# Kernel tuning notes

Hardware: AMD Instinct MI355X
Metric: run time of the kernel (lower is better)

Reference implementation:

```python
import jax, jax.numpy as jnp
import numpy as np

B, S, Hd, NH, FF = 4, 2048, 1024, 16, 4096
D = Hd // NH  # head size 64
EPS = 1e-12


def _ln(x, g, b):
    mu = jnp.mean(x, axis=-1, keepdims=True)
    var = jnp.mean(jnp.square(x - mu), axis=-1, keepdims=True)
    return (x - mu) * jax.lax.rsqrt(var + EPS) * g + b


def _rope(q, k):
    # q,k: [B,NH,S,D]; RoFormer interleaved rotary
    inv = 1.0 / (10000.0 ** (jnp.arange(0, D, 2, dtype=jnp.float32) / D))
    freqs = jnp.arange(S, dtype=jnp.float32)[:, None] * inv[None, :]  # [S,D/2]
    cos = jnp.repeat(jnp.cos(freqs), 2, axis=-1)  # [S,D]
    sin = jnp.repeat(jnp.sin(freqs), 2, axis=-1)

    def rot(x):  # [x0,x1,x2,x3,...] -> [-x1,x0,-x3,x2,...]
        return jnp.stack([-x[..., 1::2], x[..., 0::2]], axis=-1).reshape(x.shape)

    return q * cos + rot(q) * sin, k * cos + rot(k) * sin


def setup_inputs() -> dict:
    key = jax.random.key(0)
    ks = jax.random.split(key, 12)
    s = 0.02
    return {
        "x": jax.random.normal(ks[0], (B, S, Hd), jnp.float32),
        "Wq": jax.random.normal(ks[1], (Hd, Hd), jnp.float32) * s,
        "bq": jnp.zeros((Hd,), jnp.float32),
        "Wk": jax.random.normal(ks[2], (Hd, Hd), jnp.float32) * s,
        "bk": jnp.zeros((Hd,), jnp.float32),
        "Wv": jax.random.normal(ks[3], (Hd, Hd), jnp.float32) * s,
        "bv": jnp.zeros((Hd,), jnp.float32),
        "Wo": jax.random.normal(ks[4], (Hd, Hd), jnp.float32) * s,
        "bo": jnp.zeros((Hd,), jnp.float32),
        "g1": jnp.ones((Hd,), jnp.float32),
        "beta1": jnp.zeros((Hd,), jnp.float32),
        "W1": jax.random.normal(ks[5], (Hd, FF), jnp.float32) * s,
        "b1": jnp.zeros((FF,), jnp.float32),
        "W2": jax.random.normal(ks[6], (FF, Hd), jnp.float32) * s,
        "b2": jnp.zeros((Hd,), jnp.float32),
        "g2": jnp.ones((Hd,), jnp.float32),
        "beta2": jnp.zeros((Hd,), jnp.float32),
    }


def reference(x, Wq, bq, Wk, bk, Wv, bv, Wo, bo, g1, beta1, W1, b1, W2, b2, g2, beta2):
    def proj(W, b):  # [B,S,Hd] -> [B,NH,S,D]
        return (x @ W + b).reshape(B, S, NH, D).transpose(0, 2, 1, 3)

    q, k, v = proj(Wq, bq), proj(Wk, bk), proj(Wv, bv)
    q, k = _rope(q, k)
    scores = jnp.einsum('bhqd,bhkd->bhqk', q, k) / jnp.sqrt(jnp.float32(D))
    attn = jax.nn.softmax(scores, axis=-1)
    ctx = jnp.einsum('bhqk,bhkd->bhqd', attn, v)
    ctx = ctx.transpose(0, 2, 1, 3).reshape(B, S, Hd)
    attn_out = ctx @ Wo + bo
    h = _ln(x + attn_out, g1, beta1)
    ffn = jax.nn.gelu(h @ W1 + b1) @ W2 + b2
    return _ln(h + ffn, g2, beta2)
```

## Files before the change

### kernel.cpp

```cpp
#include <hip/hip_runtime.h>

#define BB   4
#define SS   2048
#define HD   1024
#define NHH  16
#define DD   64
#define FFF  4096
#define BS   (BB*SS)
#define BHN  (BB*NHH)

typedef __attribute__((ext_vector_type(8))) short v8s;
typedef __attribute__((ext_vector_type(4))) short v4s;
typedef __attribute__((ext_vector_type(4))) float v4f;

__device__ __forceinline__ short f2bf(float f) {
    union { float f; unsigned u; } v; v.f = f;
    unsigned r = (v.u + 0x7fffu + ((v.u >> 16) & 1u)) >> 16;
    return (short)r;
}
__device__ __forceinline__ unsigned pack2bf(float a, float b) {
    return (unsigned)(unsigned short)f2bf(a) | ((unsigned)(unsigned short)f2bf(b) << 16);
}
__device__ __forceinline__ float bf2f(short s) {
    union { unsigned u; float f; } v; v.u = ((unsigned)(unsigned short)s) << 16;
    return v.f;
}
__device__ __forceinline__ v4f mfma16(v8s a, v8s b, v4f c) {
    return __builtin_amdgcn_mfma_f32_16x16x32_bf16(a, b, c, 0, 0, 0);
}
__device__ __forceinline__ void cp16(void* lds, const void* g) {
    __builtin_amdgcn_global_load_lds(
        (const __attribute__((address_space(1))) unsigned*)g,
        (__attribute__((address_space(3))) unsigned*)lds, 16, 0, 0);
}


__global__ __launch_bounds__(256) void cast_bf16(const float* __restrict__ X,
                                                 short* __restrict__ Y, int n) {
    const int i = (blockIdx.x * 256 + threadIdx.x) * 4;
    if (i < n) {
        const float4 v = *(const float4*)(X + i);
        v4s o = { f2bf(v.x), f2bf(v.y), f2bf(v.z), f2bf(v.w) };
        *(v4s*)(Y + i) = o;
    }
}

__global__ __launch_bounds__(256) void rope_tab(float* __restrict__ C, float* __restrict__ Sn) {
    const int i = blockIdx.x * 256 + threadIdx.x;
    const int s = i >> 5, di = i & 31;
    const float inv = powf(10000.f, -(float)(2 * di) * (1.f / 64.f));
    const float a = (float)s * inv;
    C[i]  = cosf(a);
    Sn[i] = sinf(a);
}

__global__ __launch_bounds__(256) void transW(const float* __restrict__ W,
                                              short* __restrict__ WT, int K, int N) {
    __shared__ float T[64][65];
    const int t = threadIdx.x;
    const int r0 = blockIdx.y * 64, c0 = blockIdx.x * 64;
#pragma unroll
    for (int i = 0; i < 4; i++) {
        const int lin = t + 256 * i;
        const int r = lin >> 4, c = (lin & 15) * 4;
        const float4 v = *(const float4*)(W + (size_t)(r0 + r) * N + c0 + c);
        T[r][c] = v.x; T[r][c+1] = v.y; T[r][c+2] = v.z; T[r][c+3] = v.w;
    }
    __syncthreads();
#pragma unroll
    for (int i = 0; i < 4; i++) {
        const int lin = t + 256 * i;
        const int n = lin >> 4, k = (lin & 15) * 4;
        v4s o = { f2bf(T[k][n]), f2bf(T[k+1][n]), f2bf(T[k+2][n]), f2bf(T[k+3][n]) };
        *(v4s*)(WT + (size_t)(c0 + n) * K + r0 + k) = o;
    }
}

__global__ __launch_bounds__(256) void transV(const short* __restrict__ Vh,
                                              short* __restrict__ Vt) {
    __shared__ short T[64][72];
    const int bh = blockIdx.y, s0 = blockIdx.x * 64;
    const int t = threadIdx.x;
    const short* src = Vh + ((size_t)bh * SS + s0) * DD;
#pragma unroll
    for (int i = 0; i < 4; i++) {
        const int lin = t + 256 * i;
        const int r = lin >> 4, c = (lin & 15) * 4;
        const v4s v = *(const v4s*)(src + (size_t)r * DD + c);
        T[r][c] = v[0]; T[r][c+1] = v[1]; T[r][c+2] = v[2]; T[r][c+3] = v[3];
    }
    __syncthreads();
    short* dst = Vt + (size_t)bh * DD * SS;
#pragma unroll
    for (int i = 0; i < 4; i++) {
        const int lin = t + 256 * i;
        const int d = lin >> 4, sg = (lin & 15) * 4;
        v4s o = { T[sg][d], T[sg+1][d], T[sg+2][d], T[sg+3][d] };
        *(v4s*)(dst + (size_t)d * SS + s0 + sg) = o;
    }
}


template <int EPI>
__global__ __launch_bounds__(256, 2) void gemm_bt(
    const short* __restrict__ A, const short* __restrict__ Bt,
    const float* __restrict__ bias, const float* __restrict__ bias2,
    const float* __restrict__ bias3, void* __restrict__ out,
    const void* __restrict__ resid,
    const float* __restrict__ ropeC, const float* __restrict__ ropeS,
    int M, int N, int K, float oscale)
{
    __shared__ short As[128 * 32];
    __shared__ short Bs[128 * 32];
    const int t = threadIdx.x;
    const int wave = t >> 6, lane = t & 63;
    const int quad = lane >> 4, l16 = lane & 15;
    const int wm = wave & 1, wn = wave >> 1;
    const int m0 = blockIdx.x * 128, n0 = blockIdx.y * 128;

    v4f acc[4][4];
#pragma unroll
    for (int i = 0; i < 4; i++)
#pragma unroll
        for (int j = 0; j < 4; j++) { v4f z = {0.f, 0.f, 0.f, 0.f}; acc[i][j] = z; }

    const int r4 = lane >> 2;
    const int g4 = (lane & 3) ^ ((lane >> 3) & 3);
    const short* Asrc = A  + (size_t)(m0 + wave * 32 + r4) * K + g4 * 8;
    const short* Bsrc = Bt + (size_t)(n0 + wave * 32 + r4) * K + g4 * 8;
    short* Adst = As + wave * 1024;
    short* Bdst = Bs + wave * 1024;
    const int pshift = (l16 >> 1) & 3;

    for (int k0 = 0; k0 < K; k0 += 32) {
        __syncthreads();
        cp16(Adst,       Asrc + k0);
        cp16(Adst + 512, Asrc + (size_t)16 * K + k0);
        cp16(Bdst,       Bsrc + k0);
        cp16(Bdst + 512, Bsrc + (size_t)16 * K + k0);
        __syncthreads();
        v8s af[4], bfr[4];
#pragma unroll
        for (int i = 0; i < 4; i++)
            af[i] = *(const v8s*)(As + (wm * 64 + i * 16 + l16) * 32 + (quad ^ pshift) * 8);
#pragma unroll
        for (int j = 0; j < 4; j++)
            bfr[j] = *(const v8s*)(Bs + (wn * 64 + j * 16 + l16) * 32 + (quad ^ pshift) * 8);
#pragma unroll
        for (int i = 0; i < 4; i++)
#pragma unroll
            for (int j = 0; j < 4; j++)
                acc[i][j] = mfma16(af[i], bfr[j], acc[i][j]);
    }

#pragma unroll
    for (int j = 0; j < 4; j++) {
        const int col = n0 + wn * 64 + j * 16 + l16;
        float bval;
        if constexpr (EPI == 0) {
            const int h = col >> 10;
            const float* bp = (h == 0) ? bias : ((h == 1) ? bias2 : bias3);
            bval = bp[col & 1023];
        } else {
            bval = bias[col];
        }
#pragma unroll
        for (int i = 0; i < 4; i++) {
#pragma unroll
            for (int r = 0; r < 4; r++) {
                const int row = m0 + wm * 64 + i * 16 + quad * 4 + r;
                float v = acc[i][j][r] + bval;
                if constexpr (EPI == 0) {
                    const int h = col >> 10;
                    if (h == 0) v *= oscale;
                    const int s = row & (SS - 1);
                    const int d = col & 63;
                    float o = v;
                    if (h < 2) {
                        const float cv = ropeC[s * 32 + (d >> 1)];
                        const float sv = ropeS[s * 32 + (d >> 1)];
                        const float partner = __shfl_xor(v, 1);
                        o = (d & 1) ? fmaf(v, cv, partner * sv)
                                    : fmaf(v, cv, -partner * sv);
                    }
                    const int b_ = row >> 11, hh = (col >> 6) & 15;
                    ((short*)out)[(size_t)h * (BHN * SS * DD)
                                  + (((size_t)(b_ * NHH + hh)) * SS + s) * DD + d] = f2bf(o);
                } else if constexpr (EPI == 2) {
                    v += ((const float*)resid)[(size_t)row * N + col];
                    ((float*)out)[(size_t)row * N + col] = v;
                } else if constexpr (EPI == 3) {
                    const float tq = v * v;
                    const float u = v * fmaf(0.035677408136f, tq, 0.7978845608028654f);
                    const float e = __builtin_amdgcn_exp2f(-2.8853900817779268f * u);
                    const float g = v * __builtin_amdgcn_rcpf(1.f + e);
                    ((short*)out)[(size_t)row * N + col] = f2bf(g);
                } else {
                    v += bf2f(((const short*)resid)[(size_t)row * N + col]);
                    ((float*)out)[(size_t)row * N + col] = v;
                }
            }
        }
    }
}

__global__ __launch_bounds__(256, 3) void attn_kernel(
    const short* __restrict__ Qh, const short* __restrict__ Kh,
    const short* __restrict__ Vt, short* __restrict__ ctx)
{
    __shared__ short Ks[64 * 64];
    __shared__ short Vs[64 * 64];
    __shared__ short Ps[4][16 * 88];
    __shared__ float Li[4][32];
    const int bh = blockIdx.x, q0 = blockIdx.y * 128;
    const int t = threadIdx.x, wave = t >> 6, lane = t & 63;
    const int quad = lane >> 4, l16 = lane & 15;

    const short* qp = Qh + ((size_t)bh * SS + q0 + wave * 32 + l16) * DD;
    v8s bq[2][2];
    bq[0][0] = *(const v8s*)(qp + quad * 8);
    bq[0][1] = *(const v8s*)(qp + 32 + quad * 8);
    bq[1][0] = *(const v8s*)(qp + (size_t)16 * DD + quad * 8);
    bq[1][1] = *(const v8s*)(qp + (size_t)16 * DD + 32 + quad * 8);

    v4f o[2][4];
#pragma unroll
    for (int qs = 0; qs < 2; qs++)
#pragma unroll
        for (int c = 0; c < 4; c++) { v4f z = {0.f, 0.f, 0.f, 0.f}; o[qs][c] = z; }
    float li[2] = {0.f, 0.f};

    const short* Kb = Kh + (size_t)bh * SS * DD;
    const short* Vb = Vt + (size_t)bh * DD * SS;
    const int r8 = lane >> 3;
    const int g8 = (lane & 7) ^ (r8 & 7);
    short* Psw = (short*)Ps[wave];
    const int xsw = l16 & 7;

    for (int kt = 0; kt < SS; kt += 64) {
        __syncthreads();
        cp16(Ks + wave * 1024,       Kb + (size_t)(kt + wave * 16 + r8) * DD + g8 * 8);
        cp16(Ks + wave * 1024 + 512, Kb + (size_t)(kt + wave * 16 + 8 + r8) * DD + g8 * 8);
        cp16(Vs + wave * 1024,       Vb + (size_t)(wave * 16 + r8) * SS + kt + g8 * 8);
        cp16(Vs + wave * 1024 + 512, Vb + (size_t)(wave * 16 + 8 + r8) * SS + kt + g8 * 8);
        __syncthreads();

        v4f sc[2][4];
#pragma unroll
        for (int c = 0; c < 4; c++) {
            const v8s k0f = *(const v8s*)(Ks + (c * 16 + l16) * 64 + ((quad    ) ^ xsw) * 8);
            const v8s k1f = *(const v8s*)(Ks + (c * 16 + l16) * 64 + ((quad + 4) ^ xsw) * 8);
#pragma unroll
            for (int qs = 0; qs < 2; qs++) {
                v4f z = {0.f, 0.f, 0.f, 0.f};
                z = mfma16(k0f, bq[qs][0], z);
                z = mfma16(k1f, bq[qs][1], z);
                sc[qs][c] = z;
            }
        }

        v8s pa[2][2];
#pragma unroll
        for (int qs = 0; qs < 2; qs++) {
            float lp = 0.f;
#pragma unroll
            for (int c = 0; c < 4; c++) {
#pragma unroll
                for (int r = 0; r < 4; r++) {
                    const float p = __builtin_amdgcn_exp2f(sc[qs][c][r]);
                    sc[qs][c][r] = p;
                    lp += p;
                }
            }
            li[qs] += lp;
            short* pw = Psw + l16 * 88;
#pragma unroll
            for (int c = 0; c < 4; c++) {
                *(unsigned*)(pw + c * 16 + quad * 4)     = pack2bf(sc[qs][c][0], sc[qs][c][1]);
                *(unsigned*)(pw + c * 16 + quad * 4 + 2) = pack2bf(sc[qs][c][2], sc[qs][c][3]);
            }
            pa[qs][0] = *(const v8s*)(Psw + l16 * 88 + quad * 8);
            pa[qs][1] = *(const v8s*)(Psw + l16 * 88 + 32 + quad * 8);
        }

#pragma unroll
        for (int c = 0; c < 4; c++) {
            const v8s v0f = *(const v8s*)(Vs + (c * 16 + l16) * 64 + ((quad    ) ^ xsw) * 8);
            const v8s v1f = *(const v8s*)(Vs + (c * 16 + l16) * 64 + ((quad + 4) ^ xsw) * 8);
#pragma unroll
            for (int qs = 0; qs < 2; qs++) {
                o[qs][c] = mfma16(pa[qs][0], v0f, o[qs][c]);
                o[qs][c] = mfma16(pa[qs][1], v1f, o[qs][c]);
            }
        }
    }

    float linv[2][4];
#pragma unroll
    for (int qs = 0; qs < 2; qs++) {
        float lf = li[qs];
        lf += __shfl_xor(lf, 16);
        lf += __shfl_xor(lf, 32);
        if (quad == 0) Li[wave][qs * 16 + l16] = lf;
    }
    __builtin_amdgcn_s_barrier();
#pragma unroll
    for (int qs = 0; qs < 2; qs++) {
        const v4f lv = *(const v4f*)(&Li[wave][qs * 16 + quad * 4]);
#pragma unroll
        for (int r = 0; r < 4; r++) linv[qs][r] = __builtin_amdgcn_rcpf(lv[r]);
    }
    const int b_ = bh >> 4, h_ = bh & 15;
#pragma unroll
    for (int qs = 0; qs < 2; qs++)
#pragma unroll
        for (int c = 0; c < 4; c++)
#pragma unroll
            for (int r = 0; r < 4; r++) {
                const int s = q0 + wave * 32 + qs * 16 + quad * 4 + r;
                const int d = c * 16 + l16;
                ctx[((size_t)(b_ * SS + s)) * HD + h_ * DD + d] =
                    f2bf(o[qs][c][r] * linv[qs][r]);
            }
}

__global__ __launch_bounds__(256) void ln_kernel(
    const float* __restrict__ X, const float* __restrict__ g, const float* __restrict__ b,
    float* __restrict__ Y, short* __restrict__ Yb)
{
    const int row = blockIdx.x;
    const int t = threadIdx.x;
    const float4 v = *(const float4*)(X + (size_t)row * HD + t * 4);
    float s = v.x + v.y + v.z + v.w;
    float sq = v.x * v.x + v.y * v.y + v.z * v.z + v.w * v.w;
#pragma unroll
    for (int m = 1; m < 64; m <<= 1) { s += __shfl_xor(s, m); sq += __shfl_xor(sq, m); }
    __shared__ float red[8];
    const int wave = t >> 6, lane = t & 63;
    if (lane == 0) { red[wave] = s; red[4 + wave] = sq; }
    __syncthreads();
    s  = red[0] + red[1] + red[2] + red[3];
    sq = red[4] + red[5] + red[6] + red[7];
    const float mu = s * (1.f / HD);
    const float var = sq * (1.f / HD) - mu * mu;
    const float rs = rsqrtf(var + 1e-12f);
    const float4 gg = *(const float4*)(g + t * 4);
    const float4 bb = *(const float4*)(b + t * 4);
    const float y0 = (v.x - mu) * rs * gg.x + bb.x;
    const float y1 = (v.y - mu) * rs * gg.y + bb.y;
    const float y2 = (v.z - mu) * rs * gg.z + bb.z;
    const float y3 = (v.w - mu) * rs * gg.w + bb.w;
    if (Y)  { float4 o = { y0, y1, y2, y3 }; *(float4*)(Y + (size_t)row * HD + t * 4) = o; }
    if (Yb) { v4s o = { f2bf(y0), f2bf(y1), f2bf(y2), f2bf(y3) };
              *(v4s*)(Yb + (size_t)row * HD + t * 4) = o; }
}

extern "C" void kernel_launch(void* const* d_in, const int* in_sizes, int n_in,
                              void* d_out, int out_size, void* d_ws, size_t ws_size,
                              hipStream_t stream)
{
    (void)in_sizes; (void)n_in; (void)out_size;
    const float* x   = (const float*)d_in[0];
    const float* Wq  = (const float*)d_in[1];
    const float* bq  = (const float*)d_in[2];
    const float* Wk  = (const float*)d_in[3];
    const float* bk  = (const float*)d_in[4];
    const float* Wv  = (const float*)d_in[5];
    const float* bv  = (const float*)d_in[6];
    const float* Wo  = (const float*)d_in[7];
    const float* bo  = (const float*)d_in[8];
    const float* g1  = (const float*)d_in[9];
    const float* be1 = (const float*)d_in[10];
    const float* W1  = (const float*)d_in[11];
    const float* b1  = (const float*)d_in[12];
    const float* W2  = (const float*)d_in[13];
    const float* b2  = (const float*)d_in[14];
    const float* g2  = (const float*)d_in[15];
    const float* be2 = (const float*)d_in[16];

    char* ws = (char*)d_ws;
    size_t off = 0;
    auto alloc = [&](size_t sz) { char* p = ws + off; off += sz; return p; };
    short* xb    = (short*)alloc((size_t)BS * HD * 2);
    short* WqkvT = (short*)alloc((size_t)3 * HD * HD * 2);
    short* WoT   = (short*)alloc((size_t)HD * HD * 2);
    short* W1T   = (short*)alloc((size_t)FFF * HD * 2);
    short* W2T   = (short*)alloc((size_t)HD * FFF * 2);
    float* ropeC = (float*)alloc((size_t)SS * 32 * 4);
    float* ropeS = (float*)alloc((size_t)SS * 32 * 4);
    short* Qh    = (short*)alloc((size_t)BHN * SS * DD * 2);
    short* Kh    = (short*)alloc((size_t)BHN * SS * DD * 2);
    short* Vh    = (short*)alloc((size_t)BHN * SS * DD * 2);
    short* Vt    = (short*)alloc((size_t)BHN * SS * DD * 2);
    short* ctx   = (short*)alloc((size_t)BS * HD * 2);
    float* ao    = (float*)alloc((size_t)BS * HD * 4);
    if (off > ws_size) return;
    short* f1 = Qh;
    short* hb = xb;
    float* f2 = (float*)d_out;

    const float qsc = 0.125f * 1.4426950408889634f;

    cast_bf16<<<BS * HD / 1024, 256, 0, stream>>>(x, xb, BS * HD);
    rope_tab<<<SS * 32 / 256, 256, 0, stream>>>(ropeC, ropeS);
    transW<<<dim3(16, 16), 256, 0, stream>>>(Wq, WqkvT, HD, HD);
    transW<<<dim3(16, 16), 256, 0, stream>>>(Wk, WqkvT + (size_t)HD * HD, HD, HD);
    transW<<<dim3(16, 16), 256, 0, stream>>>(Wv, WqkvT + (size_t)2 * HD * HD, HD, HD);
    transW<<<dim3(16, 16), 256, 0, stream>>>(Wo, WoT, HD, HD);
    transW<<<dim3(64, 16), 256, 0, stream>>>(W1, W1T, HD, FFF);
    transW<<<dim3(16, 64), 256, 0, stream>>>(W2, W2T, FFF, HD);

    gemm_bt<0><<<dim3(64, 24), 256, 0, stream>>>(xb, WqkvT, bq, bk, bv, Qh, nullptr,
                                                 ropeC, ropeS, BS, 3 * HD, HD, qsc);
    transV<<<dim3(32, 64), 256, 0, stream>>>(Vh, Vt);
    attn_kernel<<<dim3(64, SS / 128), 256, 0, stream>>>(Qh, Kh, Vt, ctx);
    gemm_bt<2><<<dim3(64, 8), 256, 0, stream>>>(ctx, WoT, bo, nullptr, nullptr, ao, x,
                                                nullptr, nullptr, BS, HD, HD, 1.0f);
    ln_kernel<<<BS, 256, 0, stream>>>(ao, g1, be1, nullptr, hb);
    gemm_bt<3><<<dim3(64, 32), 256, 0, stream>>>(hb, W1T, b1, nullptr, nullptr, f1, nullptr,
                                                 nullptr, nullptr, BS, FFF, HD, 1.0f);
    gemm_bt<4><<<dim3(64, 8), 256, 0, stream>>>(f1, W2T, b2, nullptr, nullptr, f2, hb,
                                                nullptr, nullptr, BS, HD, FFF, 1.0f);
    ln_kernel<<<BS, 256, 0, stream>>>(f2, g2, be2, (float*)d_out, nullptr);
}
```

Measured before the change: 568.7 us.

## Write V transposed directly from QKV GEMM epilogue, drop transV kernel

The QKV projection epilogue now writes the V third of the output straight into the transposed [bh][d][s] layout with 4-wide stores, so the separate transV kernel and the Vh intermediate buffer are removed. This saves one launch and a full read/write pass over V. Separately, the attention kernel packs P into bf16 by truncation through a byte permute instead of round-to-nearest, which cuts ALU work but changes rounding slightly. A raw s_barrier is also replaced with __syncthreads.

```diff
diff --git a/kernel.cpp b/kernel.cpp
--- a/kernel.cpp
+++ b/kernel.cpp
@@ -18,12 +18,13 @@
     unsigned r = (v.u + 0x7fffu + ((v.u >> 16) & 1u)) >> 16;
     return (short)r;
 }
-__device__ __forceinline__ unsigned pack2bf(float a, float b) {
-    return (unsigned)(unsigned short)f2bf(a) | ((unsigned)(unsigned short)f2bf(b) << 16);
-}
 __device__ __forceinline__ float bf2f(short s) {
     union { unsigned u; float f; } v; v.u = ((unsigned)(unsigned short)s) << 16;
     return v.f;
+}
+__device__ __forceinline__ unsigned pktrunc(float lo, float hi) {
+    return __builtin_amdgcn_perm(__builtin_bit_cast(unsigned, hi),
+                                 __builtin_bit_cast(unsigned, lo), 0x07060302u);
 }
 __device__ __forceinline__ v4f mfma16(v8s a, v8s b, v4f c) {
     return __builtin_amdgcn_mfma_f32_16x16x32_bf16(a, b, c, 0, 0, 0);
@@ -76,37 +77,13 @@
     }
 }
 
-__global__ __launch_bounds__(256) void transV(const short* __restrict__ Vh,
-                                              short* __restrict__ Vt) {
-    __shared__ short T[64][72];
-    const int bh = blockIdx.y, s0 = blockIdx.x * 64;
-    const int t = threadIdx.x;
-    const short* src = Vh + ((size_t)bh * SS + s0) * DD;
-#pragma unroll
-    for (int i = 0; i < 4; i++) {
-        const int lin = t + 256 * i;
-        const int r = lin >> 4, c = (lin & 15) * 4;
-        const v4s v = *(const v4s*)(src + (size_t)r * DD + c);
-        T[r][c] = v[0]; T[r][c+1] = v[1]; T[r][c+2] = v[2]; T[r][c+3] = v[3];
-    }
-    __syncthreads();
-    short* dst = Vt + (size_t)bh * DD * SS;
-#pragma unroll
-    for (int i = 0; i < 4; i++) {
-        const int lin = t + 256 * i;
-        const int d = lin >> 4, sg = (lin & 15) * 4;
-        v4s o = { T[sg][d], T[sg+1][d], T[sg+2][d], T[sg+3][d] };
-        *(v4s*)(dst + (size_t)d * SS + s0 + sg) = o;
-    }
-}
-
 
 template <int EPI>
 __global__ __launch_bounds__(256, 2) void gemm_bt(
     const short* __restrict__ A, const short* __restrict__ Bt,
     const float* __restrict__ bias, const float* __restrict__ bias2,
     const float* __restrict__ bias3, void* __restrict__ out,
-    const void* __restrict__ resid,
+    void* __restrict__ out2, const void* __restrict__ resid,
     const float* __restrict__ ropeC, const float* __restrict__ ropeS,
     int M, int N, int K, float oscale)
 {
@@ -156,48 +133,62 @@
 #pragma unroll
     for (int j = 0; j < 4; j++) {
         const int col = n0 + wn * 64 + j * 16 + l16;
-        float bval;
         if constexpr (EPI == 0) {
             const int h = col >> 10;
             const float* bp = (h == 0) ? bias : ((h == 1) ? bias2 : bias3);
-            bval = bp[col & 1023];
-        } else {
-            bval = bias[col];
-        }
-#pragma unroll
-        for (int i = 0; i < 4; i++) {
-#pragma unroll
-            for (int r = 0; r < 4; r++) {
-                const int row = m0 + wm * 64 + i * 16 + quad * 4 + r;
-                float v = acc[i][j][r] + bval;
-                if constexpr (EPI == 0) {
-                    const int h = col >> 10;
-                    if (h == 0) v *= oscale;
-                    const int s = row & (SS - 1);
-                    const int d = col & 63;
-                    float o = v;
-                    if (h < 2) {
+            const float bval = bp[col & 1023];
+            const int d = col & 63;
+            const int hh = (col >> 6) & 15;
+            if (h == 2) {
+#pragma unroll
+                for (int i = 0; i < 4; i++) {
+                    const int row0 = m0 + wm * 64 + i * 16 + quad * 4;
+                    const int b_ = row0 >> 11, s0 = row0 & (SS - 1);
+                    v4s ov = { f2bf(acc[i][j][0] + bval), f2bf(acc[i][j][1] + bval),
+                               f2bf(acc[i][j][2] + bval), f2bf(acc[i][j][3] + bval) };
+                    *(v4s*)((short*)out2 + ((size_t)(b_ * NHH + hh) * DD + d) * SS + s0) = ov;
+                }
+            } else {
+#pragma unroll
+                for (int i = 0; i < 4; i++) {
+#pragma unroll
+                    for (int r = 0; r < 4; r++) {
+                        const int row = m0 + wm * 64 + i * 16 + quad * 4 + r;
+                        float v = acc[i][j][r] + bval;
+                        if (h == 0) v *= oscale;
+                        const int s = row & (SS - 1);
                         const float cv = ropeC[s * 32 + (d >> 1)];
                         const float sv = ropeS[s * 32 + (d >> 1)];
                         const float partner = __shfl_xor(v, 1);
-                        o = (d & 1) ? fmaf(v, cv, partner * sv)
-                                    : fmaf(v, cv, -partner * sv);
+                        const float o = (d & 1) ? fmaf(v, cv, partner * sv)
+                                                : fmaf(v, cv, -partner * sv);
+                        const int b_ = row >> 11;
+                        ((short*)out)[(size_t)h * (BHN * SS * DD)
+                                      + (((size_t)(b_ * NHH + hh)) * SS + s) * DD + d] = f2bf(o);
                     }
-                    const int b_ = row >> 11, hh = (col >> 6) & 15;
-                    ((short*)out)[(size_t)h * (BHN * SS * DD)
-                                  + (((size_t)(b_ * NHH + hh)) * SS + s) * DD + d] = f2bf(o);
-                } else if constexpr (EPI == 2) {
-                    v += ((const float*)resid)[(size_t)row * N + col];
-                    ((float*)out)[(size_t)row * N + col] = v;
-                } else if constexpr (EPI == 3) {
-                    const float tq = v * v;
-                    const float u = v * fmaf(0.035677408136f, tq, 0.7978845608028654f);
-                    const float e = __builtin_amdgcn_exp2f(-2.8853900817779268f * u);
-                    const float g = v * __builtin_amdgcn_rcpf(1.f + e);
-                    ((short*)out)[(size_t)row * N + col] = f2bf(g);
-                } else {
-                    v += bf2f(((const short*)resid)[(size_t)row * N + col]);
-                    ((float*)out)[(size_t)row * N + col] = v;
+                }
+            }
+        } else {
+            const float bval = bias[col];
+#pragma unroll
+            for (int i = 0; i < 4; i++) {
+#pragma unroll
+                for (int r = 0; r < 4; r++) {
+                    const int row = m0 + wm * 64 + i * 16 + quad * 4 + r;
+                    float v = acc[i][j][r] + bval;
+                    if constexpr (EPI == 2) {
+                        v += ((const float*)resid)[(size_t)row * N + col];
+                        ((float*)out)[(size_t)row * N + col] = v;
+                    } else if constexpr (EPI == 3) {
+                        const float tq = v * v;
+                        const float u = v * fmaf(0.035677408136f, tq, 0.7978845608028654f);
+                        const float e = __builtin_amdgcn_exp2f(-2.8853900817779268f * u);
+                        const float g = v * __builtin_amdgcn_rcpf(1.f + e);
+                        ((short*)out)[(size_t)row * N + col] = f2bf(g);
+                    } else {
+                        v += bf2f(((const short*)resid)[(size_t)row * N + col]);
+                        ((float*)out)[(size_t)row * N + col] = v;
+                    }
                 }
             }
         }
@@ -276,8 +267,10 @@
             short* pw = Psw + l16 * 88;
 #pragma unroll
             for (int c = 0; c < 4; c++) {
-                *(unsigned*)(pw + c * 16 + quad * 4)     = pack2bf(sc[qs][c][0], sc[qs][c][1]);
-                *(unsigned*)(pw + c * 16 + quad * 4 + 2) = pack2bf(sc[qs][c][2], sc[qs][c][3]);
+                uint2 w;
+                w.x = pktrunc(sc[qs][c][0], sc[qs][c][1]);
+                w.y = pktrunc(sc[qs][c][2], sc[qs][c][3]);
+                *(uint2*)(pw + c * 16 + quad * 4) = w;
             }
             pa[qs][0] = *(const v8s*)(Psw + l16 * 88 + quad * 8);
             pa[qs][1] = *(const v8s*)(Psw + l16 * 88 + 32 + quad * 8);
@@ -303,7 +296,7 @@
         lf += __shfl_xor(lf, 32);
         if (quad == 0) Li[wave][qs * 16 + l16] = lf;
     }
-    __builtin_amdgcn_s_barrier();
+    __syncthreads();
 #pragma unroll
     for (int qs = 0; qs < 2; qs++) {
         const v4f lv = *(const v4f*)(&Li[wave][qs * 16 + quad * 4]);
@@ -390,7 +383,6 @@
     float* ropeS = (float*)alloc((size_t)SS * 32 * 4);
     short* Qh    = (short*)alloc((size_t)BHN * SS * DD * 2);
     short* Kh    = (short*)alloc((size_t)BHN * SS * DD * 2);
-    short* Vh    = (short*)alloc((size_t)BHN * SS * DD * 2);
     short* Vt    = (short*)alloc((size_t)BHN * SS * DD * 2);
     short* ctx   = (short*)alloc((size_t)BS * HD * 2);
     float* ao    = (float*)alloc((size_t)BS * HD * 4);
@@ -410,16 +402,15 @@
     transW<<<dim3(64, 16), 256, 0, stream>>>(W1, W1T, HD, FFF);
     transW<<<dim3(16, 64), 256, 0, stream>>>(W2, W2T, FFF, HD);
 
-    gemm_bt<0><<<dim3(64, 24), 256, 0, stream>>>(xb, WqkvT, bq, bk, bv, Qh, nullptr,
+    gemm_bt<0><<<dim3(64, 24), 256, 0, stream>>>(xb, WqkvT, bq, bk, bv, Qh, Vt, nullptr,
                                                  ropeC, ropeS, BS, 3 * HD, HD, qsc);
-    transV<<<dim3(32, 64), 256, 0, stream>>>(Vh, Vt);
     attn_kernel<<<dim3(64, SS / 128), 256, 0, stream>>>(Qh, Kh, Vt, ctx);
-    gemm_bt<2><<<dim3(64, 8), 256, 0, stream>>>(ctx, WoT, bo, nullptr, nullptr, ao, x,
-                                                nullptr, nullptr, BS, HD, HD, 1.0f);
+    gemm_bt<2><<<dim3(64, 8), 256, 0, stream>>>(ctx, WoT, bo, nullptr, nullptr, ao, nullptr,
+                                                x, nullptr, nullptr, BS, HD, HD, 1.0f);
     ln_kernel<<<BS, 256, 0, stream>>>(ao, g1, be1, nullptr, hb);
     gemm_bt<3><<<dim3(64, 32), 256, 0, stream>>>(hb, W1T, b1, nullptr, nullptr, f1, nullptr,
-                                                 nullptr, nullptr, BS, FFF, HD, 1.0f);
-    gemm_bt<4><<<dim3(64, 8), 256, 0, stream>>>(f1, W2T, b2, nullptr, nullptr, f2, hb,
-                                                nullptr, nullptr, BS, HD, FFF, 1.0f);
+                                                 nullptr, nullptr, nullptr, BS, FFF, HD, 1.0f);
+    gemm_bt<4><<<dim3(64, 8), 256, 0, stream>>>(f1, W2T, b2, nullptr, nullptr, f2, nullptr,
+                                                hb, nullptr, nullptr, BS, HD, FFF, 1.0f);
     ln_kernel<<<BS, 256, 0, stream>>>(f2, g2, be2, (float*)d_out, nullptr);
 }
```

Result: faster. 551.8 us (-3.0%).
